# Performance work log

Hardware: AMD Instinct MI355X
Metric: run time of the kernel (lower is better)

Reference implementation:

```python
import jax, jax.numpy as jnp
import numpy as np
import math

B, S, E, H, D = 2, 2048, 1024, 16, 64

def setup_inputs() -> dict:
    key = jax.random.key(0)
    ks = jax.random.split(key, 9)
    sc = 0.02
    return {
        "x": jax.random.normal(ks[0], (B, S, E), jnp.float32),
        "Wq": jax.random.normal(ks[1], (H, E, D), jnp.float32) * sc,
        "Wk": jax.random.normal(ks[2], (H, E, D), jnp.float32) * sc,
        "Wv": jax.random.normal(ks[3], (H, E, D), jnp.float32) * sc,
        "bq": jax.random.normal(ks[4], (H, D), jnp.float32) * sc,
        "bk": jax.random.normal(ks[5], (H, D), jnp.float32) * sc,
        "bv": jax.random.normal(ks[6], (H, D), jnp.float32) * sc,
        "Wo": jax.random.normal(ks[7], (H * D, E), jnp.float32) * sc,
        "bo": jax.random.normal(ks[8], (E,), jnp.float32) * sc,
    }

def reference(x, Wq, Wk, Wv, bq, bk, bv, Wo, bo):
    # per-head projections, batched over heads: [B,H,S,D]
    q = jnp.einsum('bse,hed->bhsd', x, Wq) + bq[None, :, None, :]
    k = jnp.einsum('bse,hed->bhsd', x, Wk) + bk[None, :, None, :]
    v = jnp.einsum('bse,hed->bhsd', x, Wv) + bv[None, :, None, :]
    # full score matrix [B,H,S,S], scaled by sqrt(head_size) as in original
    scores = jnp.einsum('bhqd,bhkd->bhqk', q, k) / math.sqrt(D)
    causal = jnp.tril(jnp.ones((S, S), bool))  # tril mask as in buffer
    scores = jnp.where(causal[None, None], scores, -jnp.inf)
    attn = jax.nn.softmax(scores, axis=-1)
    out = jnp.einsum('bhqk,bhkd->bhqd', attn, v)
    # concat heads in head order: [B,S,H*D]
    out = out.transpose(0, 2, 1, 3).reshape(B, S, H * D)
    # output projection (dropout is identity in eval / p=0)
    return out @ Wo + bo
```

## Files before the change

### kernel.cpp

```cpp
#include <hip/hip_runtime.h>

#define BB 2
#define SS 2048
#define EE 1024
#define HH 16
#define DD 64

typedef unsigned short u16;
typedef float f4 __attribute__((ext_vector_type(4)));
typedef __bf16 b8 __attribute__((ext_vector_type(8)));
typedef short s8i __attribute__((ext_vector_type(8)));
typedef u16 u16x4 __attribute__((ext_vector_type(4)));

__device__ inline u16 f2b(float f) {
  unsigned u = __builtin_bit_cast(unsigned, f);
  unsigned r = (u + 0x7fffu + ((u >> 16) & 1u)) >> 16;
  return (u16)r;
}

__global__ void castx(const float* __restrict__ x, u16* __restrict__ xb) {
  const int N4 = BB * SS * EE / 4;
  for (int i = blockIdx.x * blockDim.x + threadIdx.x; i < N4;
       i += gridDim.x * blockDim.x) {
    f4 v = ((const f4*)x)[i];
    u16x4 o;
    for (int j = 0; j < 4; ++j) o[j] = f2b(v[j]);
    ((u16x4*)xb)[i] = o;
  }
}

__global__ __launch_bounds__(256) void transW(const float* __restrict__ Wq,
                                              const float* __restrict__ Wk,
                                              const float* __restrict__ Wv,
                                              u16* __restrict__ Wt) {
  __shared__ float tile[64][65];
  int t = threadIdx.x;
  int e0 = blockIdx.x * 64;
  int y = blockIdx.y;
  int qkv = y >> 4, h = y & 15;
  const float* W = (qkv == 0) ? Wq : (qkv == 1) ? Wk : Wv;
  for (int p = 0; p < 16; ++p) {
    int i = p * 4 + (t >> 6), d = t & 63;
    tile[i][d] = W[((size_t)h * EE + e0 + i) * DD + d];
  }
  __syncthreads();
  for (int p = 0; p < 16; ++p) {
    int d = p * 4 + (t >> 6), i = t & 63;
    Wt[((size_t)qkv * 1024 + h * 64 + d) * EE + e0 + i] = f2b(tile[i][d]);
  }
}

__global__ __launch_bounds__(256) void transWo(const float* __restrict__ Wo,
                                               u16* __restrict__ Wot) {
  __shared__ float tile[64][65];
  int t = threadIdx.x;
  int e0 = blockIdx.x * 64, c0 = blockIdx.y * 64;
  for (int p = 0; p < 16; ++p) {
    int i = p * 4 + (t >> 6), j = t & 63;
    tile[i][j] = Wo[(size_t)(e0 + i) * (HH * DD) + c0 + j];
  }
  __syncthreads();
  for (int p = 0; p < 16; ++p) {
    int j = p * 4 + (t >> 6), i = t & 63;
    Wot[(size_t)(c0 + j) * EE + e0 + i] = f2b(tile[i][j]);
  }
}

template <int MODE>
__global__ __launch_bounds__(256) void gemm128(
    const u16* __restrict__ A, const u16* __restrict__ Bm,
    u16* __restrict__ Qo, u16* __restrict__ Ko, u16* __restrict__ Vo,
    const float* __restrict__ bq, const float* __restrict__ bk,
    const float* __restrict__ bv,
    float* __restrict__ Co, const float* __restrict__ bo) {
  const int K = 1024;
  __shared__ u16 As[128 * 32];
  __shared__ u16 Bs[128 * 32];
  int t = threadIdx.x;
  int lane = t & 63, w = t >> 6;
  int wr = w >> 1, wc = w & 1;
  int lr = lane & 15, lg = lane >> 4;
  int m0 = blockIdx.y * 128, n0 = blockIdx.x * 128;

  f4 acc[4][4];
  const f4 z4 = {0.f, 0.f, 0.f, 0.f};
  for (int mi = 0; mi < 4; ++mi)
    for (int ni = 0; ni < 4; ++ni) acc[mi][ni] = z4;

  int r0 = t >> 2, s0 = t & 3;
  const u16* ga0 = A + (size_t)(m0 + r0) * K + s0 * 8;
  const u16* gb0 = Bm + (size_t)(n0 + r0) * K + s0 * 8;
  u16* la0 = As + w * 512;
  u16* la1 = As + 2048 + w * 512;
  u16* lb0 = Bs + w * 512;
  u16* lb1 = Bs + 2048 + w * 512;

  for (int ks = 0; ks < K / 32; ++ks) {
    int k0 = ks * 32;
    __builtin_amdgcn_global_load_lds(
        (const __attribute__((address_space(1))) void*)(ga0 + k0),
        (__attribute__((address_space(3))) void*)la0, 16, 0, 0);
    __builtin_amdgcn_global_load_lds(
        (const __attribute__((address_space(1))) void*)(ga0 + 64 * K + k0),
        (__attribute__((address_space(3))) void*)la1, 16, 0, 0);
    __builtin_amdgcn_global_load_lds(
        (const __attribute__((address_space(1))) void*)(gb0 + k0),
        (__attribute__((address_space(3))) void*)lb0, 16, 0, 0);
    __builtin_amdgcn_global_load_lds(
        (const __attribute__((address_space(1))) void*)(gb0 + 64 * K + k0),
        (__attribute__((address_space(3))) void*)lb1, 16, 0, 0);
    __syncthreads();
    b8 af[4], bf[4];
    for (int mi = 0; mi < 4; ++mi)
      af[mi] = *(const b8*)&As[(wr * 64 + mi * 16 + lr) * 32 + lg * 8];
    for (int ni = 0; ni < 4; ++ni)
      bf[ni] = *(const b8*)&Bs[(wc * 64 + ni * 16 + lr) * 32 + lg * 8];
    for (int mi = 0; mi < 4; ++mi)
      for (int ni = 0; ni < 4; ++ni)
        acc[mi][ni] = __builtin_amdgcn_mfma_f32_16x16x32_bf16(af[mi], bf[ni],
                                                              acc[mi][ni], 0, 0, 0);
    __syncthreads();
  }

  for (int mi = 0; mi < 4; ++mi)
    for (int ni = 0; ni < 4; ++ni)
      for (int r = 0; r < 4; ++r) {
        int m_g = m0 + wr * 64 + mi * 16 + lg * 4 + r;
        int n_g = n0 + wc * 64 + ni * 16 + lr;
        float v = acc[mi][ni][r];
        if (MODE == 0) {
          int qkv = n_g >> 10, hd = n_g & 1023;
          const float* bias = (qkv == 0) ? bq : (qkv == 1) ? bk : bv;
          v += bias[hd];
          int b = m_g >> 11, s = m_g & 2047;
          int h = hd >> 6, d = hd & 63;
          if (qkv == 0) {
            Qo[(((size_t)b * HH + h) * SS + s) * DD + d] = f2b(v * 0.125f);
          } else if (qkv == 1) {
            Ko[(((size_t)b * HH + h) * SS + s) * DD + d] = f2b(v);
          } else {
            Vo[(((size_t)b * HH + h) * DD + d) * SS + s] = f2b(v);
          }
        } else {
          Co[(size_t)m_g * 1024 + n_g] = v + bo[n_g];
        }
      }
}

#define KST 72
#define PST 72
__global__ __launch_bounds__(256) void fattn(const u16* __restrict__ Qb,
                                             const u16* __restrict__ Kb,
                                             const u16* __restrict__ VTb,
                                             u16* __restrict__ AO) {
  __shared__ u16 Kl[2][64 * KST];
  __shared__ u16 Pl[4][16 * PST];

  int t = threadIdx.x, lane = t & 63, w = t >> 6;
  int lr = lane & 15, lg = lane >> 4;
  int bh = blockIdx.y;
  int b = bh >> 4, h = bh & 15;
  size_t base = (size_t)bh * SS * DD;

  int r0 = t >> 2, s0 = t & 3;
  u16* kl0 = &Kl[0][r0 * KST + s0 * 8];
  u16* kl1 = &Kl[1][r0 * KST + s0 * 8];
  const u16* kg = Kb + base + (size_t)r0 * DD + s0 * 8;

  for (int half = 0; half < 2; ++half) {
    int qt = half ? blockIdx.x : 31 - blockIdx.x;
    int qbase = qt * 64;
    int nt = qt + 1;

    const u16* qp = Qb + base + (size_t)(qbase + w * 16 + lr) * DD;
    b8 qf0 = *(const b8*)(qp + lg * 8);
    b8 qf1 = *(const b8*)(qp + 32 + lg * 8);

    const f4 z4 = {0.f, 0.f, 0.f, 0.f};
    f4 o[4];
    for (int i = 0; i < 4; ++i) o[i] = z4;
    float mrow[4], lsum[4];
    for (int r = 0; r < 4; ++r) { mrow[r] = -1e30f; lsum[r] = 0.f; }
    int qg = qbase + w * 16 + lg * 4;

    {
      s8i k0v = *(const s8i*)(kg);
      s8i k1v = *(const s8i*)(kg + 32);
      *(s8i*)kl0 = k0v;
      *(s8i*)(kl0 + 32) = k1v;
    }
    __syncthreads();

    for (int kt = 0; kt < nt; ++kt) {
      int cur = kt & 1;
      int kv0 = kt * 64;
      const u16* vp = VTb + base + kv0 + (size_t)lr * SS;

      b8 vr[8];
      for (int n = 0; n < 4; ++n) {
        vr[2 * n] = *(const b8*)(vp + (size_t)(n * 16) * SS + lg * 8);
        vr[2 * n + 1] = *(const b8*)(vp + (size_t)(n * 16) * SS + 32 + lg * 8);
      }
      s8i nk0, nk1;
      bool more = (kt + 1 < nt);
      if (more) {
        const u16* kgn = kg + (size_t)(kv0 + 64) * DD;
        nk0 = *(const s8i*)(kgn);
        nk1 = *(const s8i*)(kgn + 32);
      }

      f4 sa[4];
      for (int n = 0; n < 4; ++n) sa[n] = z4;
      for (int n = 0; n < 4; ++n) {
        b8 kf0 = *(const b8*)&Kl[cur][(n * 16 + lr) * KST + lg * 8];
        b8 kf1 = *(const b8*)&Kl[cur][(n * 16 + lr) * KST + 32 + lg * 8];
        sa[n] = __builtin_amdgcn_mfma_f32_16x16x32_bf16(qf0, kf0, sa[n], 0, 0, 0);
        sa[n] = __builtin_amdgcn_mfma_f32_16x16x32_bf16(qf1, kf1, sa[n], 0, 0, 0);
      }

      bool diag = (kt == nt - 1);
      float scl[4];
      for (int r = 0; r < 4; ++r) {
        float v0 = sa[0][r], v1 = sa[1][r], v2 = sa[2][r], v3 = sa[3][r];
        if (diag) {
          int q = qg + r;
          if (kv0 + lr > q) v0 = -1e30f;
          if (kv0 + 16 + lr > q) v1 = -1e30f;
          if (kv0 + 32 + lr > q) v2 = -1e30f;
          if (kv0 + 48 + lr > q) v3 = -1e30f;
        }
        float mx = fmaxf(fmaxf(v0, v1), fmaxf(v2, v3));
        mx = fmaxf(mx, __shfl_xor(mx, 1));
        mx = fmaxf(mx, __shfl_xor(mx, 2));
        mx = fmaxf(mx, __shfl_xor(mx, 4));
        mx = fmaxf(mx, __shfl_xor(mx, 8));
        float mn = fmaxf(mrow[r], mx);
        float sc = __expf(mrow[r] - mn);
        float p0 = __expf(v0 - mn), p1 = __expf(v1 - mn);
        float p2 = __expf(v2 - mn), p3 = __expf(v3 - mn);
        float ps = (p0 + p1) + (p2 + p3);
        ps += __shfl_xor(ps, 1);
        ps += __shfl_xor(ps, 2);
        ps += __shfl_xor(ps, 4);
        ps += __shfl_xor(ps, 8);
        lsum[r] = lsum[r] * sc + ps;
        mrow[r] = mn;
        scl[r] = sc;
        int prow = (lg * 4 + r) * PST;
        Pl[w][prow + lr] = f2b(p0);
        Pl[w][prow + 16 + lr] = f2b(p1);
        Pl[w][prow + 32 + lr] = f2b(p2);
        Pl[w][prow + 48 + lr] = f2b(p3);
      }
      for (int n = 0; n < 4; ++n) {
        f4 ov = o[n];
        for (int r = 0; r < 4; ++r) ov[r] *= scl[r];
        o[n] = ov;
      }

      b8 pf0 = *(const b8*)&Pl[w][lr * PST + lg * 8];
      b8 pf1 = *(const b8*)&Pl[w][lr * PST + 32 + lg * 8];
      for (int n = 0; n < 4; ++n) {
        o[n] = __builtin_amdgcn_mfma_f32_16x16x32_bf16(pf0, vr[2 * n], o[n], 0, 0, 0);
        o[n] = __builtin_amdgcn_mfma_f32_16x16x32_bf16(pf1, vr[2 * n + 1], o[n], 0, 0, 0);
      }

      if (more) {
        u16* kln = cur ? kl0 : kl1;
        *(s8i*)kln = nk0;
        *(s8i*)(kln + 32) = nk1;
      }
      __syncthreads();
    }

    for (int n = 0; n < 4; ++n)
      for (int r = 0; r < 4; ++r) {
        int qgr = qg + r;
        int d = n * 16 + lr;
        float val = o[n][r] / lsum[r];
        AO[((size_t)b * SS + qgr) * (HH * DD) + h * DD + d] = f2b(val);
      }
    __syncthreads();
  }
}

extern "C" void kernel_launch(void* const* d_in, const int* in_sizes, int n_in,
                              void* d_out, int out_size, void* d_ws, size_t ws_size,
                              hipStream_t stream) {
  const float* x  = (const float*)d_in[0];
  const float* Wq = (const float*)d_in[1];
  const float* Wk = (const float*)d_in[2];
  const float* Wv = (const float*)d_in[3];
  const float* bq = (const float*)d_in[4];
  const float* bk = (const float*)d_in[5];
  const float* bv = (const float*)d_in[6];
  const float* Wo = (const float*)d_in[7];
  const float* bo = (const float*)d_in[8];

  char* ws = (char*)d_ws;
  u16* xb  = (u16*)(ws);
  u16* Wt  = (u16*)(ws + ((size_t)8 << 20));
  u16* Wot = (u16*)(ws + ((size_t)14 << 20));
  u16* Qw  = (u16*)(ws + ((size_t)16 << 20));
  u16* Kw  = (u16*)(ws + ((size_t)24 << 20));
  u16* VTw = (u16*)(ws + ((size_t)32 << 20));
  u16* AO  = xb;

  castx<<<1024, 256, 0, stream>>>(x, xb);
  transW<<<dim3(16, 48), 256, 0, stream>>>(Wq, Wk, Wv, Wt);
  transWo<<<dim3(16, 16), 256, 0, stream>>>(Wo, Wot);
  gemm128<0><<<dim3(24, 32), 256, 0, stream>>>(xb, Wt, Qw, Kw, VTw, bq, bk, bv,
                                               nullptr, nullptr);
  fattn<<<dim3(16, 32), 256, 0, stream>>>(Qw, Kw, VTw, AO);
  gemm128<1><<<dim3(8, 32), 256, 0, stream>>>(AO, Wot, nullptr, nullptr, nullptr,
                                              nullptr, nullptr, nullptr,
                                              (float*)d_out, bo);
}
```

Baseline: 238.6 us.

## Merge prep kernels, stage V through LDS, use exp2 softmax with deferred row-sum reduction

Combines the three preprocessing kernels (x cast, QKV weight transpose, Wo transpose) into one launch, dispatching on block index. In the attention kernel, V tiles are now double-buffered in shared memory alongside K instead of being read per-wave straight from global memory. The softmax uses exp2 with log2(e) folded into the Q scale. The per-tile cross-lane row-sum shuffle is replaced by a single reduction at the end, and the final division becomes a multiply by a reciprocal. The extra LDS for V may reduce occupancy, and bf16 rounding of Q now includes the log2(e) factor.

```diff
diff --git a/kernel.cpp b/kernel.cpp
--- a/kernel.cpp
+++ b/kernel.cpp
@@ -18,51 +18,54 @@
   return (u16)r;
 }
 
-__global__ void castx(const float* __restrict__ x, u16* __restrict__ xb) {
-  const int N4 = BB * SS * EE / 4;
-  for (int i = blockIdx.x * blockDim.x + threadIdx.x; i < N4;
-       i += gridDim.x * blockDim.x) {
-    f4 v = ((const f4*)x)[i];
-    u16x4 o;
-    for (int j = 0; j < 4; ++j) o[j] = f2b(v[j]);
-    ((u16x4*)xb)[i] = o;
-  }
-}
-
-__global__ __launch_bounds__(256) void transW(const float* __restrict__ Wq,
-                                              const float* __restrict__ Wk,
-                                              const float* __restrict__ Wv,
-                                              u16* __restrict__ Wt) {
-  __shared__ float tile[64][65];
+__global__ __launch_bounds__(256) void prep(const float* __restrict__ x,
+                                            const float* __restrict__ Wq,
+                                            const float* __restrict__ Wk,
+                                            const float* __restrict__ Wv,
+                                            const float* __restrict__ Wo,
+                                            u16* __restrict__ xb,
+                                            u16* __restrict__ Wt,
+                                            u16* __restrict__ Wot) {
+  int bid = blockIdx.x;
   int t = threadIdx.x;
-  int e0 = blockIdx.x * 64;
-  int y = blockIdx.y;
-  int qkv = y >> 4, h = y & 15;
-  const float* W = (qkv == 0) ? Wq : (qkv == 1) ? Wk : Wv;
-  for (int p = 0; p < 16; ++p) {
-    int i = p * 4 + (t >> 6), d = t & 63;
-    tile[i][d] = W[((size_t)h * EE + e0 + i) * DD + d];
-  }
-  __syncthreads();
-  for (int p = 0; p < 16; ++p) {
-    int d = p * 4 + (t >> 6), i = t & 63;
-    Wt[((size_t)qkv * 1024 + h * 64 + d) * EE + e0 + i] = f2b(tile[i][d]);
-  }
-}
-
-__global__ __launch_bounds__(256) void transWo(const float* __restrict__ Wo,
-                                               u16* __restrict__ Wot) {
-  __shared__ float tile[64][65];
-  int t = threadIdx.x;
-  int e0 = blockIdx.x * 64, c0 = blockIdx.y * 64;
-  for (int p = 0; p < 16; ++p) {
-    int i = p * 4 + (t >> 6), j = t & 63;
-    tile[i][j] = Wo[(size_t)(e0 + i) * (HH * DD) + c0 + j];
-  }
-  __syncthreads();
-  for (int p = 0; p < 16; ++p) {
-    int j = p * 4 + (t >> 6), i = t & 63;
-    Wot[(size_t)(c0 + j) * EE + e0 + i] = f2b(tile[i][j]);
+  if (bid < 1024) {
+    int i0 = bid * 256 + t;
+    for (int j = 0; j < 4; ++j) {
+      int i = i0 + j * 262144;
+      f4 v = ((const f4*)x)[i];
+      u16x4 o;
+      for (int k2 = 0; k2 < 4; ++k2) o[k2] = f2b(v[k2]);
+      ((u16x4*)xb)[i] = o;
+    }
+  } else if (bid < 1792) {
+    __shared__ float tile[64][65];
+    int z = bid - 1024;
+    int y = z >> 4;
+    int e0 = (z & 15) * 64;
+    int qkv = y >> 4, h = y & 15;
+    const float* W = (qkv == 0) ? Wq : (qkv == 1) ? Wk : Wv;
+    for (int p = 0; p < 16; ++p) {
+      int i = p * 4 + (t >> 6), d = t & 63;
+      tile[i][d] = W[((size_t)h * EE + e0 + i) * DD + d];
+    }
+    __syncthreads();
+    for (int p = 0; p < 16; ++p) {
+      int d = p * 4 + (t >> 6), i = t & 63;
+      Wt[((size_t)qkv * 1024 + h * 64 + d) * EE + e0 + i] = f2b(tile[i][d]);
+    }
+  } else {
+    __shared__ float tile2[64][65];
+    int z = bid - 1792;
+    int e0 = (z & 15) * 64, c0 = (z >> 4) * 64;
+    for (int p = 0; p < 16; ++p) {
+      int i = p * 4 + (t >> 6), j = t & 63;
+      tile2[i][j] = Wo[(size_t)(e0 + i) * (HH * DD) + c0 + j];
+    }
+    __syncthreads();
+    for (int p = 0; p < 16; ++p) {
+      int j = p * 4 + (t >> 6), i = t & 63;
+      Wot[(size_t)(c0 + j) * EE + e0 + i] = f2b(tile2[i][j]);
+    }
   }
 }
 
@@ -122,6 +125,7 @@
     __syncthreads();
   }
 
+  const float QSC = 0.18033688011112042f;
   for (int mi = 0; mi < 4; ++mi)
     for (int ni = 0; ni < 4; ++ni)
       for (int r = 0; r < 4; ++r) {
@@ -135,7 +139,7 @@
           int b = m_g >> 11, s = m_g & 2047;
           int h = hd >> 6, d = hd & 63;
           if (qkv == 0) {
-            Qo[(((size_t)b * HH + h) * SS + s) * DD + d] = f2b(v * 0.125f);
+            Qo[(((size_t)b * HH + h) * SS + s) * DD + d] = f2b(v * QSC);
           } else if (qkv == 1) {
             Ko[(((size_t)b * HH + h) * SS + s) * DD + d] = f2b(v);
           } else {
@@ -154,6 +158,7 @@
                                              const u16* __restrict__ VTb,
                                              u16* __restrict__ AO) {
   __shared__ u16 Kl[2][64 * KST];
+  __shared__ u16 Vl[2][64 * KST];
   __shared__ u16 Pl[4][16 * PST];
 
   int t = threadIdx.x, lane = t & 63, w = t >> 6;
@@ -165,7 +170,10 @@
   int r0 = t >> 2, s0 = t & 3;
   u16* kl0 = &Kl[0][r0 * KST + s0 * 8];
   u16* kl1 = &Kl[1][r0 * KST + s0 * 8];
+  u16* vl0 = &Vl[0][r0 * KST + s0 * 8];
+  u16* vl1 = &Vl[1][r0 * KST + s0 * 8];
   const u16* kg = Kb + base + (size_t)r0 * DD + s0 * 8;
+  const u16* vg = VTb + base + (size_t)r0 * SS + s0 * 8;
 
   for (int half = 0; half < 2; ++half) {
     int qt = half ? blockIdx.x : 31 - blockIdx.x;
@@ -184,29 +192,26 @@
     int qg = qbase + w * 16 + lg * 4;
 
     {
-      s8i k0v = *(const s8i*)(kg);
-      s8i k1v = *(const s8i*)(kg + 32);
-      *(s8i*)kl0 = k0v;
-      *(s8i*)(kl0 + 32) = k1v;
+      *(s8i*)kl0 = *(const s8i*)(kg);
+      *(s8i*)(kl0 + 32) = *(const s8i*)(kg + 32);
+      *(s8i*)vl0 = *(const s8i*)(vg);
+      *(s8i*)(vl0 + 32) = *(const s8i*)(vg + 32);
     }
     __syncthreads();
 
     for (int kt = 0; kt < nt; ++kt) {
       int cur = kt & 1;
       int kv0 = kt * 64;
-      const u16* vp = VTb + base + kv0 + (size_t)lr * SS;
-
-      b8 vr[8];
-      for (int n = 0; n < 4; ++n) {
-        vr[2 * n] = *(const b8*)(vp + (size_t)(n * 16) * SS + lg * 8);
-        vr[2 * n + 1] = *(const b8*)(vp + (size_t)(n * 16) * SS + 32 + lg * 8);
-      }
-      s8i nk0, nk1;
+
+      s8i nk0, nk1, nv0, nv1;
       bool more = (kt + 1 < nt);
       if (more) {
         const u16* kgn = kg + (size_t)(kv0 + 64) * DD;
+        const u16* vgn = vg + kv0 + 64;
         nk0 = *(const s8i*)(kgn);
         nk1 = *(const s8i*)(kgn + 32);
+        nv0 = *(const s8i*)(vgn);
+        nv1 = *(const s8i*)(vgn + 32);
       }
 
       f4 sa[4];
@@ -218,32 +223,30 @@
         sa[n] = __builtin_amdgcn_mfma_f32_16x16x32_bf16(qf1, kf1, sa[n], 0, 0, 0);
       }
 
-      bool diag = (kt == nt - 1);
+      if (kt == nt - 1) {
+        for (int r = 0; r < 4; ++r) {
+          int q = qg + r;
+          if (kv0 + lr > q) sa[0][r] = -1e30f;
+          if (kv0 + 16 + lr > q) sa[1][r] = -1e30f;
+          if (kv0 + 32 + lr > q) sa[2][r] = -1e30f;
+          if (kv0 + 48 + lr > q) sa[3][r] = -1e30f;
+        }
+      }
+
       float scl[4];
       for (int r = 0; r < 4; ++r) {
-        float v0 = sa[0][r], v1 = sa[1][r], v2 = sa[2][r], v3 = sa[3][r];
-        if (diag) {
-          int q = qg + r;
-          if (kv0 + lr > q) v0 = -1e30f;
-          if (kv0 + 16 + lr > q) v1 = -1e30f;
-          if (kv0 + 32 + lr > q) v2 = -1e30f;
-          if (kv0 + 48 + lr > q) v3 = -1e30f;
-        }
-        float mx = fmaxf(fmaxf(v0, v1), fmaxf(v2, v3));
+        float mx = fmaxf(fmaxf(sa[0][r], sa[1][r]), fmaxf(sa[2][r], sa[3][r]));
         mx = fmaxf(mx, __shfl_xor(mx, 1));
         mx = fmaxf(mx, __shfl_xor(mx, 2));
         mx = fmaxf(mx, __shfl_xor(mx, 4));
         mx = fmaxf(mx, __shfl_xor(mx, 8));
         float mn = fmaxf(mrow[r], mx);
-        float sc = __expf(mrow[r] - mn);
-        float p0 = __expf(v0 - mn), p1 = __expf(v1 - mn);
-        float p2 = __expf(v2 - mn), p3 = __expf(v3 - mn);
-        float ps = (p0 + p1) + (p2 + p3);
-        ps += __shfl_xor(ps, 1);
-        ps += __shfl_xor(ps, 2);
-        ps += __shfl_xor(ps, 4);
-        ps += __shfl_xor(ps, 8);
-        lsum[r] = lsum[r] * sc + ps;
+        float sc = __builtin_amdgcn_exp2f(mrow[r] - mn);
+        float p0 = __builtin_amdgcn_exp2f(sa[0][r] - mn);
+        float p1 = __builtin_amdgcn_exp2f(sa[1][r] - mn);
+        float p2 = __builtin_amdgcn_exp2f(sa[2][r] - mn);
+        float p3 = __builtin_amdgcn_exp2f(sa[3][r] - mn);
+        lsum[r] = lsum[r] * sc + ((p0 + p1) + (p2 + p3));
         mrow[r] = mn;
         scl[r] = sc;
         int prow = (lg * 4 + r) * PST;
@@ -261,24 +264,37 @@
       b8 pf0 = *(const b8*)&Pl[w][lr * PST + lg * 8];
       b8 pf1 = *(const b8*)&Pl[w][lr * PST + 32 + lg * 8];
       for (int n = 0; n < 4; ++n) {
-        o[n] = __builtin_amdgcn_mfma_f32_16x16x32_bf16(pf0, vr[2 * n], o[n], 0, 0, 0);
-        o[n] = __builtin_amdgcn_mfma_f32_16x16x32_bf16(pf1, vr[2 * n + 1], o[n], 0, 0, 0);
+        b8 vf0 = *(const b8*)&Vl[cur][(n * 16 + lr) * KST + lg * 8];
+        b8 vf1 = *(const b8*)&Vl[cur][(n * 16 + lr) * KST + 32 + lg * 8];
+        o[n] = __builtin_amdgcn_mfma_f32_16x16x32_bf16(pf0, vf0, o[n], 0, 0, 0);
+        o[n] = __builtin_amdgcn_mfma_f32_16x16x32_bf16(pf1, vf1, o[n], 0, 0, 0);
       }
 
       if (more) {
         u16* kln = cur ? kl0 : kl1;
+        u16* vln = cur ? vl0 : vl1;
         *(s8i*)kln = nk0;
         *(s8i*)(kln + 32) = nk1;
+        *(s8i*)vln = nv0;
+        *(s8i*)(vln + 32) = nv1;
       }
       __syncthreads();
     }
 
+    float rl[4];
+    for (int r = 0; r < 4; ++r) {
+      float s = lsum[r];
+      s += __shfl_xor(s, 1);
+      s += __shfl_xor(s, 2);
+      s += __shfl_xor(s, 4);
+      s += __shfl_xor(s, 8);
+      rl[r] = 1.f / s;
+    }
     for (int n = 0; n < 4; ++n)
       for (int r = 0; r < 4; ++r) {
         int qgr = qg + r;
         int d = n * 16 + lr;
-        float val = o[n][r] / lsum[r];
-        AO[((size_t)b * SS + qgr) * (HH * DD) + h * DD + d] = f2b(val);
+        AO[((size_t)b * SS + qgr) * (HH * DD) + h * DD + d] = f2b(o[n][r] * rl[r]);
       }
     __syncthreads();
   }
@@ -306,9 +322,7 @@
   u16* VTw = (u16*)(ws + ((size_t)32 << 20));
   u16* AO  = xb;
 
-  castx<<<1024, 256, 0, stream>>>(x, xb);
-  transW<<<dim3(16, 48), 256, 0, stream>>>(Wq, Wk, Wv, Wt);
-  transWo<<<dim3(16, 16), 256, 0, stream>>>(Wo, Wot);
+  prep<<<2048, 256, 0, stream>>>(x, Wq, Wk, Wv, Wo, xb, Wt, Wot);
   gemm128<0><<<dim3(24, 32), 256, 0, stream>>>(xb, Wt, Qw, Kw, VTw, bq, bk, bv,
                                                nullptr, nullptr);
   fattn<<<dim3(16, 32), 256, 0, stream>>>(Qw, Kw, VTw, AO);
```

Result: faster. 221.3 us (-7.3%).
